# Kernel tuning notes

Measured on AMD Instinct MI355X. Metric: run time of the kernel, lower is better.

Reference implementation:

```python
import jax, jax.numpy as jnp
import numpy as np

K = 3    # spline degree
NUM = 5  # grid intervals


def _extended_grid(in_dim):
    # pykan default grid_range=[-1,1], extended by K knots of spacing h on each side
    h = 2.0 / NUM
    g = jnp.linspace(-1.0 - K * h, 1.0 + K * h, NUM + 2 * K + 1, dtype=jnp.float32)
    return jnp.tile(g[None, :], (in_dim, 1))  # (in_dim, NUM+2K+1)


def _bspline_basis(x, grid):
    # Cox-de Boor recursion, matches pykan B_batch.
    # x: (..., in_dim); grid: (in_dim, NUM+2K+1) -> (..., in_dim, NUM+K)
    xe = x[..., None]
    B = ((xe >= grid[:, :-1]) & (xe < grid[:, 1:])).astype(x.dtype)
    for d in range(1, K + 1):
        left = (xe - grid[:, :-(d + 1)]) / (grid[:, d:-1] - grid[:, :-(d + 1)])
        right = (grid[:, d + 1:] - xe) / (grid[:, d + 1:] - grid[:, 1:-d])
        B = left * B[..., :-1] + right * B[..., 1:]
    return B


def _kan_layer(x, grid, coef, scale_base, scale_sp):
    # pykan KANLayer.forward (mask == 1): y = sum_i scale_base*silu(x) + scale_sp*spline(x)
    base = jax.nn.silu(x)                              # (..., in)
    Bx = _bspline_basis(x, grid)                       # (..., in, NUM+K)
    spl = jnp.einsum('...ik,iok->...io', Bx, coef)     # (..., in, out)
    y = scale_base * base[..., None] + scale_sp * spl  # (..., in, out)
    return y.sum(axis=-2)                              # (..., out)


def setup_inputs() -> dict:
    key = jax.random.key(0)
    seq_len, in_dim, hidden_dim, out_dim = 8192, 128, 512, 128
    nb = NUM + K
    hu_in = in_dim + hidden_dim
    ks = jax.random.split(key, 5)
    return {
        "x": jax.random.normal(ks[0], (seq_len, in_dim), jnp.float32),
        "h0": jnp.zeros((hidden_dim,), jnp.float32),
        "hu_grid": _extended_grid(hu_in),
        "hu_coef": jax.random.normal(ks[1], (hu_in, hidden_dim, nb), jnp.float32) * 0.1,
        "hu_scale_base": jax.random.normal(ks[2], (hu_in, hidden_dim), jnp.float32) / np.sqrt(hu_in).astype(np.float32),
        "hu_scale_sp": jnp.ones((hu_in, hidden_dim), jnp.float32) / np.float32(np.sqrt(hu_in)),
        "out_grid": _extended_grid(hidden_dim),
        "out_coef": jax.random.normal(ks[3], (hidden_dim, out_dim, nb), jnp.float32) * 0.1,
        "out_scale_base": jax.random.normal(ks[4], (hidden_dim, out_dim), jnp.float32) / np.float32(np.sqrt(hidden_dim)),
        "out_scale_sp": jnp.ones((hidden_dim, out_dim), jnp.float32) / np.float32(np.sqrt(hidden_dim)),
    }


def reference(x, h0, hu_grid, hu_coef, hu_scale_base, hu_scale_sp,
              out_grid, out_coef, out_scale_base, out_scale_sp):
    # Sequential KAN-cell recurrence over time (torch for-loop -> lax.scan)
    def step(h, x_t):
        inp = jnp.concatenate([x_t, h])  # (in_dim + hidden_dim,)
        h_new = _kan_layer(inp, hu_grid, hu_coef, hu_scale_base, hu_scale_sp)
        return h_new, h_new

    _, hidden_states = jax.lax.scan(step, h0, x)  # (seq, hidden)
    outputs = _kan_layer(hidden_states, out_grid, out_coef, out_scale_base, out_scale_sp)
    return outputs, hidden_states
```

## Files before the change

kernel.cpp:

```cpp
#include <hip/hip_runtime.h>
#include <math.h>

#define SEQ 8192
#define IN_DIM 128
#define HID 512
#define OUT_DIM 128
#define NK 9
#define KNOTS 12

#define WS_W9HU  0
#define WS_WSEQ  589824
#define WS_XPART (WS_WSEQ + 2359296)
#define WS_HCOMM (WS_XPART + 4194304)
#define WS_TOTAL (WS_HCOMM + 4194304)

#define SENTINEL 0x7FA0DEADu

#define NWG 32
#define TPB2 512

__device__ __forceinline__ int brow(int ib) { return ib*3 + (ib >> 4); }

__device__ __forceinline__ void load_knots(const float* gptr, float* g, float* invA) {
    #pragma unroll
    for (int j = 0; j < KNOTS; ++j) g[j] = gptr[j];
    #pragma unroll
    for (int d = 1; d <= 3; ++d) {
        #pragma unroll
        for (int j = 0; j < 11; ++j) {
            if (j + d <= 11) invA[(d-1)*11 + j] = 1.0f / (g[j+d] - g[j]);
        }
    }
}

__device__ __forceinline__ void basis9(float x, const float* g, const float* invA, float* out) {
    float B[11];
    #pragma unroll
    for (int j = 0; j < 11; ++j)
        B[j] = (x >= g[j] && x < g[j+1]) ? 1.0f : 0.0f;
    #pragma unroll
    for (int d = 1; d <= 3; ++d) {
        #pragma unroll
        for (int j = 0; j < 11; ++j) {
            if (j + d < 11) {
                float left  = (x - g[j]) * invA[(d-1)*11 + j];
                float right = (g[j+d+1] - x) * invA[(d-1)*11 + j + 1];
                B[j] = left * B[j] + right * B[j+1];
            }
        }
    }
    #pragma unroll
    for (int j = 0; j < 8; ++j) out[j] = B[j];
    out[8] = x / (1.0f + expf(-x));
}

__global__ __launch_bounds__(256) void build1_kernel(
    const float* __restrict__ hu_coef, const float* __restrict__ hu_sb, const float* __restrict__ hu_ssp,
    float* __restrict__ ws)
{
    int idx = blockIdx.x * blockDim.x + threadIdx.x;
    int stride = gridDim.x * blockDim.x;
    const int N1 = 128 * 9 * 512;
    for (int p = idx; p < N1; p += stride) {
        int o = p & 511; int k = (p >> 9) % 9; int i = p / 4608;
        float v = (k < 8) ? hu_ssp[i*HID + o] * hu_coef[(i*HID + o)*8 + k] : hu_sb[i*HID + o];
        ws[WS_W9HU + p] = v;
    }
    const int N2 = 32 * 128 * 4 * 4 * 4 * 9;
    for (int p = idx; p < N2; p += stride) {
        int k = p % 9; int rest = p / 9;
        int j = rest & 3; rest >>= 2;
        int r = rest & 3; rest >>= 2;
        int oq = rest & 3; rest >>= 2;
        int q = rest & 127; int blk = rest >> 7;
        int gi = IN_DIM + 4*q + r;
        int o  = blk*16 + oq*4 + j;
        float v = (k < 8) ? hu_ssp[gi*HID + o] * hu_coef[(gi*HID + o)*8 + k] : hu_sb[gi*HID + o];
        ws[WS_WSEQ + p] = v;
    }
    unsigned* hc = (unsigned*)(ws + WS_HCOMM);
    for (int p = idx; p < SEQ*HID; p += stride) hc[p] = SENTINEL;
}

__global__ __launch_bounds__(256) void build2_kernel(
    const float* __restrict__ out_coef, const float* __restrict__ out_sb, const float* __restrict__ out_ssp,
    float* __restrict__ ws)
{
    int idx = blockIdx.x * blockDim.x + threadIdx.x;
    int stride = gridDim.x * blockDim.x;
    const int N = 512 * 9 * 128;
    for (int p = idx; p < N; p += stride) {
        int o = p & 127; int k = (p >> 7) % 9; int i = p / 1152;
        float v = (k < 8) ? out_ssp[i*OUT_DIM + o] * out_coef[(i*OUT_DIM + o)*8 + k] : out_sb[i*OUT_DIM + o];
        ws[WS_W9HU + p] = v;
    }
}

#define R1 4
__global__ __launch_bounds__(256) void xpart_kernel(
    const float* __restrict__ X, const float* __restrict__ hu_grid, float* __restrict__ ws)
{
    const int tid = threadIdx.x;
    const int t0 = blockIdx.x * R1;
    const float* W9 = ws + WS_W9HU;
    float* xpart = ws + WS_XPART;
    float g[KNOTS], invA[33];
    load_knots(hu_grid, g, invA);

    __shared__ float4 bas4[R1*IN_DIM*3 + (R1*IN_DIM)/16];
    #pragma unroll
    for (int rep = 0; rep < 2; ++rep) {
        int idx = tid + rep*256;
        int r = idx >> 7, i = idx & 127;
        float bv[9];
        basis9(X[(t0 + r)*IN_DIM + i], g, invA, bv);
        int rb = brow(idx);
        bas4[rb]   = make_float4(bv[0], bv[1], bv[2], bv[3]);
        bas4[rb+1] = make_float4(bv[4], bv[5], bv[6], bv[7]);
        bas4[rb+2] = make_float4(bv[8], 0.f, 0.f, 0.f);
    }
    __syncthreads();

    float acc[R1][2];
    #pragma unroll
    for (int r = 0; r < R1; ++r) { acc[r][0] = 0.f; acc[r][1] = 0.f; }

    for (int i = 0; i < IN_DIM; ++i) {
        float w1[9], w2[9];
        #pragma unroll
        for (int k = 0; k < 9; ++k) {
            w1[k] = W9[(i*NK+k)*HID + tid];
            w2[k] = W9[(i*NK+k)*HID + tid + 256];
        }
        #pragma unroll
        for (int r = 0; r < R1; ++r) {
            const float* rp = (const float*)&bas4[brow(r*IN_DIM + i)];
            float4 b0 = ((const float4*)rp)[0], b1 = ((const float4*)rp)[1];
            float b8 = rp[8];
            float s1 = w1[0]*b0.x + w1[1]*b0.y + w1[2]*b0.z + w1[3]*b0.w
                     + w1[4]*b1.x + w1[5]*b1.y + w1[6]*b1.z + w1[7]*b1.w + w1[8]*b8;
            float s2 = w2[0]*b0.x + w2[1]*b0.y + w2[2]*b0.z + w2[3]*b0.w
                     + w2[4]*b1.x + w2[5]*b1.y + w2[6]*b1.z + w2[7]*b1.w + w2[8]*b8;
            acc[r][0] += s1; acc[r][1] += s2;
        }
    }
    #pragma unroll
    for (int r = 0; r < R1; ++r) {
        xpart[(t0+r)*HID + tid]       = acc[r][0];
        xpart[(t0+r)*HID + tid + 256] = acc[r][1];
    }
}

__global__ __launch_bounds__(TPB2, 2) void seq_kernel(
    const float* __restrict__ h0, const float* __restrict__ hu_grid,
    float* __restrict__ ws, float* __restrict__ d_out)
{
    const int tid  = threadIdx.x;
    const int blk  = blockIdx.x;
    const int lane = tid & 63;
    const int wave = tid >> 6;
    const int oq   = tid & 3;
    const int q    = tid >> 2;
    const float* xpart = ws + WS_XPART;
    float* hcomm = ws + WS_HCOMM;
    float* hs_out = d_out + (size_t)SEQ*OUT_DIM;
    const float g0 = hu_grid[0];
    const float inv_h = 1.0f / (hu_grid[1] - hu_grid[0]);

    float w[4][4][9];
    {
        const float* Wb = ws + WS_WSEQ + ((size_t)((blk*128 + q)*4 + oq))*144;
        #pragma unroll
        for (int r = 0; r < 4; ++r)
            #pragma unroll
            for (int j = 0; j < 4; ++j)
                #pragma unroll
                for (int k = 0; k < 9; ++k)
                    w[r][j][k] = Wb[(r*4 + j)*9 + k];
    }

    __shared__ float4 bas4[3*HID + HID/16 + 4];
    __shared__ float red[8][4][4];

    for (int t = 0; t < SEQ; ++t) {
        float xf = (tid < 16) ? xpart[(size_t)t*HID + blk*16 + tid] : 0.0f;

        float hv;
        if (t == 0) {
            hv = h0[tid];
        } else {
            const unsigned* pp = (const unsigned*)&hcomm[(size_t)(t-1)*HID + tid];
            unsigned u = __hip_atomic_load(pp, __ATOMIC_RELAXED, __HIP_MEMORY_SCOPE_AGENT);
            int sp = 0;
            while (u == SENTINEL && ++sp < (1 << 24))
                u = __hip_atomic_load(pp, __ATOMIC_RELAXED, __HIP_MEMORY_SCOPE_AGENT);
            hv = __uint_as_float(u);
        }

        {
            float* rowp = (float*)&bas4[brow(tid)];
            float tq = (hv - g0) * inv_h;
            float cf = floorf(tq);
            float u  = tq - cf;
            int   c  = (int)cf;
            float si = hv * __builtin_amdgcn_rcpf(1.0f + __expf(-hv));
            ((float4*)rowp)[0] = make_float4(0.f, 0.f, 0.f, 0.f);
            ((float4*)rowp)[1] = make_float4(0.f, 0.f, 0.f, 0.f);
            rowp[8] = si;
            if (c >= 0 && c <= 10) {
                float um = 1.0f - u, u2 = u*u, u3 = u2*u;
                float P0 = um*um*um*(1.0f/6.0f);
                float P1 = 0.5f*u3 - u2 + (2.0f/3.0f);
                float P2 = -0.5f*u3 + 0.5f*u2 + 0.5f*u + (1.0f/6.0f);
                float P3 = u3*(1.0f/6.0f);
                int j0 = c - 3;
                if (j0     >= 0)              rowp[j0]     = P0;
                if (j0 + 1 >= 0 && j0+1 <= 7) rowp[j0 + 1] = P1;
                if (j0 + 2 >= 0 && j0+2 <= 7) rowp[j0 + 2] = P2;
                if (j0 + 3 <= 7)              rowp[j0 + 3] = P3;
            }
        }
        __syncthreads();

        float p0 = 0.f, p1 = 0.f, p2 = 0.f, p3 = 0.f;
        #pragma unroll
        for (int r = 0; r < 4; ++r) {
            int row = 4*q + r;
            const float* rp = (const float*)&bas4[brow(row)];
            float4 b0 = ((const float4*)rp)[0], b1 = ((const float4*)rp)[1];
            float b8 = rp[8];
            p0 += w[r][0][0]*b0.x + w[r][0][1]*b0.y + w[r][0][2]*b0.z + w[r][0][3]*b0.w
                + w[r][0][4]*b1.x + w[r][0][5]*b1.y + w[r][0][6]*b1.z + w[r][0][7]*b1.w + w[r][0][8]*b8;
            p1 += w[r][1][0]*b0.x + w[r][1][1]*b0.y + w[r][1][2]*b0.z + w[r][1][3]*b0.w
                + w[r][1][4]*b1.x + w[r][1][5]*b1.y + w[r][1][6]*b1.z + w[r][1][7]*b1.w + w[r][1][8]*b8;
            p2 += w[r][2][0]*b0.x + w[r][2][1]*b0.y + w[r][2][2]*b0.z + w[r][2][3]*b0.w
                + w[r][2][4]*b1.x + w[r][2][5]*b1.y + w[r][2][6]*b1.z + w[r][2][7]*b1.w + w[r][2][8]*b8;
            p3 += w[r][3][0]*b0.x + w[r][3][1]*b0.y + w[r][3][2]*b0.z + w[r][3][3]*b0.w
                + w[r][3][4]*b1.x + w[r][3][5]*b1.y + w[r][3][6]*b1.z + w[r][3][7]*b1.w + w[r][3][8]*b8;
        }
        #pragma unroll
        for (int d = 4; d < 64; d <<= 1) {
            p0 += __shfl_xor(p0, d, 64);
            p1 += __shfl_xor(p1, d, 64);
            p2 += __shfl_xor(p2, d, 64);
            p3 += __shfl_xor(p3, d, 64);
        }
        if (lane < 4) {
            red[wave][lane][0] = p0;
            red[wave][lane][1] = p1;
            red[wave][lane][2] = p2;
            red[wave][lane][3] = p3;
        }
        __syncthreads();
        if (tid < 16) {
            float s = xf;
            #pragma unroll
            for (int wv = 0; wv < 8; ++wv) s += red[wv][tid>>2][tid&3];
            __hip_atomic_store((unsigned*)&hcomm[(size_t)t*HID + blk*16 + tid], __float_as_uint(s),
                               __ATOMIC_RELAXED, __HIP_MEMORY_SCOPE_AGENT);
            hs_out[(size_t)t*HID + blk*16 + tid] = s;
        }
        __syncthreads();
    }
}

#define R3 2
__global__ __launch_bounds__(256) void outlayer_kernel(
    const float* __restrict__ out_grid, float* __restrict__ ws, float* __restrict__ d_out)
{
    const int tid = threadIdx.x;
    const int t0 = blockIdx.x * R3;
    const float* W9o = ws + WS_W9HU;
    const float* hs = d_out + (size_t)SEQ*OUT_DIM;
    float g[KNOTS], invA[33];
    load_knots(out_grid, g, invA);

    __shared__ float4 bas4[R3*HID*3 + (R3*HID)/16];
    #pragma unroll
    for (int rep = 0; rep < 4; ++rep) {
        int idx = tid + rep*256;
        int r = idx >> 9, i = idx & 511;
        float bv[9];
        basis9(hs[(size_t)(t0+r)*HID + i], g, invA, bv);
        int rb = brow(idx);
        bas4[rb]   = make_float4(bv[0], bv[1], bv[2], bv[3]);
        bas4[rb+1] = make_float4(bv[4], bv[5], bv[6], bv[7]);
        bas4[rb+2] = make_float4(bv[8], 0.f, 0.f, 0.f);
    }
    __syncthreads();

    const int oo = tid & 127;
    const int half = tid >> 7;
    float acc[R3] = {0.f, 0.f};
    for (int ii = 0; ii < 256; ++ii) {
        int i = half*256 + ii;
        float wv[9];
        #pragma unroll
        for (int k = 0; k < 9; ++k) wv[k] = W9o[(i*NK+k)*OUT_DIM + oo];
        #pragma unroll
        for (int r = 0; r < R3; ++r) {
            const float* rp = (const float*)&bas4[brow(r*HID + i)];
            float4 b0 = ((const float4*)rp)[0], b1 = ((const float4*)rp)[1];
            float b8 = rp[8];
            acc[r] += wv[0]*b0.x + wv[1]*b0.y + wv[2]*b0.z + wv[3]*b0.w
                    + wv[4]*b1.x + wv[5]*b1.y + wv[6]*b1.z + wv[7]*b1.w + wv[8]*b8;
        }
    }
    __shared__ float red[2][R3][128];
    red[half][0][oo] = acc[0];
    red[half][1][oo] = acc[1];
    __syncthreads();
    {
        int rr = tid >> 7, o2 = tid & 127;
        d_out[(size_t)(t0+rr)*OUT_DIM + o2] = red[0][rr][o2] + red[1][rr][o2];
    }
}

extern "C" void kernel_launch(void* const* d_in, const int* in_sizes, int n_in,
                              void* d_out, int out_size, void* d_ws, size_t ws_size,
                              hipStream_t stream) {
    (void)in_sizes; (void)n_in; (void)out_size; (void)ws_size;
    const float* X        = (const float*)d_in[0];
    const float* h0       = (const float*)d_in[1];
    const float* hu_grid  = (const float*)d_in[2];
    const float* hu_coef  = (const float*)d_in[3];
    const float* hu_sb    = (const float*)d_in[4];
    const float* hu_ssp   = (const float*)d_in[5];
    const float* out_grid = (const float*)d_in[6];
    const float* out_coef = (const float*)d_in[7];
    const float* out_sb   = (const float*)d_in[8];
    const float* out_ssp  = (const float*)d_in[9];
    float* out = (float*)d_out;
    float* ws  = (float*)d_ws;

    hipLaunchKernelGGL(build1_kernel, dim3(2048), dim3(256), 0, stream,
                       hu_coef, hu_sb, hu_ssp, ws);
    hipLaunchKernelGGL(xpart_kernel, dim3(SEQ/R1), dim3(256), 0, stream, X, hu_grid, ws);
    hipLaunchKernelGGL(seq_kernel, dim3(NWG), dim3(TPB2), 0, stream, h0, hu_grid, ws, out);
    hipLaunchKernelGGL(build2_kernel, dim3(1024), dim3(256), 0, stream,
                       out_coef, out_sb, out_ssp, ws);
    hipLaunchKernelGGL(outlayer_kernel, dim3(SEQ/R3), dim3(256), 0, stream, out_grid, ws, out);
}
```

Before: 16.79 ms.

## Elect all sequential workgroups onto one XCC and use lighter cross-block polling

Launches 512 workgroups and, through an atomic election that favours XCC 0, keeps 32 of them running the recurrence. When all 32 land on the same XCC it polls the hidden-state handoff with sc0 loads, which can be served from that XCC's shared L2 instead of device-scope atomics. This targets the per-step cross-workgroup latency of the serial scan. It also changes the LDS basis layout to a 12-float stride with an XOR swizzle. The election adds a startup spin and extra launched blocks, and it relies on XCC placement behaviour and on writes becoming visible within the XCC.

```diff
diff --git a/kernel.cpp b/kernel.cpp
--- a/kernel.cpp
+++ b/kernel.cpp
@@ -8,18 +8,29 @@
 #define NK 9
 #define KNOTS 12
 
-#define WS_W9HU  0
-#define WS_WSEQ  589824
+#define WS_ELECT 0
+#define WS_W9HU  64
+#define WS_WSEQ  (WS_W9HU + 589824)
 #define WS_XPART (WS_WSEQ + 2359296)
 #define WS_HCOMM (WS_XPART + 4194304)
 #define WS_TOTAL (WS_HCOMM + 4194304)
 
 #define SENTINEL 0x7FA0DEADu
+#define SLOT_INIT 0xFFFFFFFFu
 
 #define NWG 32
 #define TPB2 512
+#define NB_LAUNCH 512
 
 __device__ __forceinline__ int brow(int ib) { return ib*3 + (ib >> 4); }
+__device__ __forceinline__ int rho(int i) { return i ^ ((i >> 4) & 7); }
+
+__device__ __forceinline__ unsigned ld_sc0(const unsigned* p) {
+    unsigned r;
+    asm volatile("global_load_dword %0, %1, off sc0\n\ts_waitcnt vmcnt(0)"
+                 : "=v"(r) : "v"(p) : "memory");
+    return r;
+}
 
 __device__ __forceinline__ void load_knots(const float* gptr, float* g, float* invA) {
     #pragma unroll
@@ -60,6 +71,8 @@
 {
     int idx = blockIdx.x * blockDim.x + threadIdx.x;
     int stride = gridDim.x * blockDim.x;
+    if (idx == 0) ((unsigned*)ws)[0] = 0u;
+    else if (idx <= 32) ((unsigned*)ws)[idx] = SLOT_INIT;
     const int N1 = 128 * 9 * 512;
     for (int p = idx; p < N1; p += stride) {
         int o = p & 511; int k = (p >> 9) % 9; int i = p / 4608;
@@ -151,12 +164,51 @@
     }
 }
 
-__global__ __launch_bounds__(TPB2, 2) void seq_kernel(
+__global__ __launch_bounds__(TPB2, 1) void seq_kernel(
     const float* __restrict__ h0, const float* __restrict__ hu_grid,
     float* __restrict__ ws, float* __restrict__ d_out)
 {
-    const int tid  = threadIdx.x;
-    const int blk  = blockIdx.x;
+    __shared__ int sh_slot, sh_mode;
+    __shared__ float basf[512*12];
+    __shared__ float red[8][4][4];
+
+    const int tid = threadIdx.x;
+    unsigned* el = (unsigned*)ws;
+
+    if (tid == 0) {
+        unsigned xcc;
+        asm volatile("s_getreg_b32 %0, hwreg(HW_REG_XCC_ID)" : "=s"(xcc));
+        int slot = 64;
+        if (xcc == 0u) {
+            slot = (int)__hip_atomic_fetch_add(&el[0], 1u, __ATOMIC_RELAXED, __HIP_MEMORY_SCOPE_AGENT);
+        } else {
+            unsigned long long tc0 = __builtin_amdgcn_s_memrealtime();
+            while (__builtin_amdgcn_s_memrealtime() - tc0 < 2500ull) {}
+            unsigned c = __hip_atomic_load(&el[0], __ATOMIC_RELAXED, __HIP_MEMORY_SCOPE_AGENT);
+            if (c < (unsigned)NWG)
+                slot = (int)__hip_atomic_fetch_add(&el[0], 1u, __ATOMIC_RELAXED, __HIP_MEMORY_SCOPE_AGENT);
+        }
+        int mode = 0;
+        if (slot < NWG) {
+            __hip_atomic_store(&el[1+slot], xcc, __ATOMIC_RELAXED, __HIP_MEMORY_SCOPE_AGENT);
+            int ok = 1; unsigned first = 0;
+            for (int i = 0; i < NWG; ++i) {
+                unsigned v; int sp = 0;
+                do { v = __hip_atomic_load(&el[1+i], __ATOMIC_RELAXED, __HIP_MEMORY_SCOPE_AGENT); }
+                while (v == SLOT_INIT && ++sp < (1 << 20));
+                if (v == SLOT_INIT) { ok = 0; break; }
+                if (i == 0) first = v;
+                else if (v != first) { ok = 0; break; }
+            }
+            mode = ok;
+        }
+        sh_slot = slot; sh_mode = mode;
+    }
+    __syncthreads();
+    const int blk = sh_slot;
+    const int mode = sh_mode;
+    if (blk >= NWG) return;
+
     const int lane = tid & 63;
     const int wave = tid >> 6;
     const int oq   = tid & 3;
@@ -179,9 +231,6 @@
                     w[r][j][k] = Wb[(r*4 + j)*9 + k];
     }
 
-    __shared__ float4 bas4[3*HID + HID/16 + 4];
-    __shared__ float red[8][4][4];
-
     for (int t = 0; t < SEQ; ++t) {
         float xf = (tid < 16) ? xpart[(size_t)t*HID + blk*16 + tid] : 0.0f;
 
@@ -190,15 +239,22 @@
             hv = h0[tid];
         } else {
             const unsigned* pp = (const unsigned*)&hcomm[(size_t)(t-1)*HID + tid];
-            unsigned u = __hip_atomic_load(pp, __ATOMIC_RELAXED, __HIP_MEMORY_SCOPE_AGENT);
-            int sp = 0;
-            while (u == SENTINEL && ++sp < (1 << 24))
+            unsigned u;
+            if (mode) {
+                u = ld_sc0(pp);
+                int sp = 0;
+                while (u == SENTINEL && ++sp < 64) u = ld_sc0(pp);
+            } else {
+                u = __hip_atomic_load(pp, __ATOMIC_RELAXED, __HIP_MEMORY_SCOPE_AGENT);
+            }
+            int sp2 = 0;
+            while (u == SENTINEL && ++sp2 < (1 << 24))
                 u = __hip_atomic_load(pp, __ATOMIC_RELAXED, __HIP_MEMORY_SCOPE_AGENT);
             hv = __uint_as_float(u);
         }
 
         {
-            float* rowp = (float*)&bas4[brow(tid)];
+            float* rowp = basf + rho(tid)*12;
             float tq = (hv - g0) * inv_h;
             float cf = floorf(tq);
             float u  = tq - cf;
@@ -225,8 +281,7 @@
         float p0 = 0.f, p1 = 0.f, p2 = 0.f, p3 = 0.f;
         #pragma unroll
         for (int r = 0; r < 4; ++r) {
-            int row = 4*q + r;
-            const float* rp = (const float*)&bas4[brow(row)];
+            const float* rp = basf + rho(4*q + r)*12;
             float4 b0 = ((const float4*)rp)[0], b1 = ((const float4*)rp)[1];
             float b8 = rp[8];
             p0 += w[r][0][0]*b0.x + w[r][0][1]*b0.y + w[r][0][2]*b0.z + w[r][0][3]*b0.w
@@ -256,8 +311,10 @@
             float s = xf;
             #pragma unroll
             for (int wv = 0; wv < 8; ++wv) s += red[wv][tid>>2][tid&3];
-            __hip_atomic_store((unsigned*)&hcomm[(size_t)t*HID + blk*16 + tid], __float_as_uint(s),
-                               __ATOMIC_RELAXED, __HIP_MEMORY_SCOPE_AGENT);
+            unsigned su = __float_as_uint(s);
+            unsigned* dst = (unsigned*)&hcomm[(size_t)t*HID + blk*16 + tid];
+            *(volatile unsigned*)dst = su;
+            __hip_atomic_store(dst, su, __ATOMIC_RELAXED, __HIP_MEMORY_SCOPE_AGENT);
             hs_out[(size_t)t*HID + blk*16 + tid] = s;
         }
         __syncthreads();
@@ -336,7 +393,7 @@
     hipLaunchKernelGGL(build1_kernel, dim3(2048), dim3(256), 0, stream,
                        hu_coef, hu_sb, hu_ssp, ws);
     hipLaunchKernelGGL(xpart_kernel, dim3(SEQ/R1), dim3(256), 0, stream, X, hu_grid, ws);
-    hipLaunchKernelGGL(seq_kernel, dim3(NWG), dim3(TPB2), 0, stream, h0, hu_grid, ws, out);
+    hipLaunchKernelGGL(seq_kernel, dim3(NB_LAUNCH), dim3(TPB2), 0, stream, h0, hu_grid, ws, out);
     hipLaunchKernelGGL(build2_kernel, dim3(1024), dim3(256), 0, stream,
                        out_coef, out_sb, out_ssp, ws);
     hipLaunchKernelGGL(outlayer_kernel, dim3(SEQ/R3), dim3(256), 0, stream, out_grid, ws, out);
```

Result: slower. 54.20 ms (+222.8%).
